# Optimization experiments

Measured on AMD Instinct MI355X. Metric: run time of the kernel, lower is better.

Reference implementation:

```python
import jax, jax.numpy as jnp
import numpy as np
import math

N_HEAD = 16
HEAD_DIM = 64
BASE = 10000.0

def setup_inputs() -> dict:
    key = jax.random.key(0)
    k1, k2, k3, k4 = jax.random.split(key, 4)
    B, T, C = 2, 2048, 1024
    x = jax.random.normal(k1, (B, T, C), dtype=jnp.float32)
    w_attn = jax.random.normal(k2, (3 * C, C), dtype=jnp.float32) * 0.02
    w_proj = jax.random.normal(k3, (C, C), dtype=jnp.float32) * 0.02
    delta = jax.random.normal(k4, (N_HEAD, HEAD_DIM), dtype=jnp.float32) * 0.5
    return {"x": x, "w_attn": w_attn, "w_proj": w_proj, "delta": delta}

def reference(x, w_attn, w_proj, delta):
    B, T, C = x.shape
    H, D = N_HEAD, HEAD_DIM
    # qkv projection (nn.Linear, no bias): x @ W^T
    qkv = jnp.einsum('btc,ec->bte', x, w_attn)
    q, k, v = jnp.split(qkv, 3, axis=-1)
    q = q.reshape(B, T, H, D).transpose(0, 2, 1, 3)  # (B,H,T,D)
    k = k.reshape(B, T, H, D).transpose(0, 2, 1, 3)
    v = v.reshape(B, T, H, D).transpose(0, 2, 1, 3)
    # PoPE: d frequencies per head
    inv_freq = 1.0 / (BASE ** (jnp.arange(D, dtype=jnp.float32) / D))  # (D,)
    t = jnp.arange(T, dtype=jnp.float32)
    freqs = t[:, None] * inv_freq[None, :]            # (T,D)
    cos_pos = jnp.cos(freqs)[None, None]              # (1,1,T,D)
    sin_pos = jnp.sin(freqs)[None, None]
    mu_q = jax.nn.softplus(q)
    mu_k = jax.nn.softplus(k)
    d = jnp.clip(delta, -2.0 * math.pi, 0.0)          # (H,D)
    cos_d = jnp.cos(d)[None, :, None, :]              # (1,H,1,D)
    sin_d = jnp.sin(d)[None, :, None, :]
    q_real = mu_q * cos_pos
    q_imag = mu_q * sin_pos
    k_real = mu_k * (cos_pos * cos_d - sin_pos * sin_d)
    k_imag = mu_k * (sin_pos * cos_d + cos_pos * sin_d)
    scale = 1.0 / math.sqrt(D)
    att = (jnp.einsum('bhtd,bhsd->bhts', q_real, k_real)
           + jnp.einsum('bhtd,bhsd->bhts', q_imag, k_imag)) * scale
    causal = jnp.tril(jnp.ones((T, T), dtype=bool))
    att = jnp.where(causal[None, None], att, -jnp.inf)
    att = jax.nn.softmax(att, axis=-1)
    y = jnp.einsum('bhts,bhsd->bhtd', att, v)
    y = y.transpose(0, 2, 1, 3).reshape(B, T, C)
    return jnp.einsum('btc,ec->bte', y, w_proj)
```

## Files before the change

kernel.cpp:

```cpp
#include <hip/hip_runtime.h>
#include <math.h>

typedef short s16x8 __attribute__((ext_vector_type(8)));
typedef float f32x4 __attribute__((ext_vector_type(4)));
typedef float f32x16 __attribute__((ext_vector_type(16)));
typedef unsigned short u16;

#define B_ 2
#define T_ 2048
#define HN_ 16

__device__ __forceinline__ u16 f2bf(float f) {
  union { float f; unsigned u; } v; v.f = f;
  unsigned r = v.u + 0x7FFFu + ((v.u >> 16) & 1u);
  return (u16)(r >> 16);
}
__device__ __forceinline__ float bf2f(u16 b) {
  union { unsigned u; float f; } v; v.u = ((unsigned)b) << 16;
  return v.f;
}
__device__ __forceinline__ float softplus_f(float v) {
  return fmaxf(v, 0.f) + __logf(1.f + __expf(-fabsf(v)));
}
__device__ __forceinline__ f32x4 mfma16(s16x8 a, s16x8 b, f32x4 c) {
  return __builtin_amdgcn_mfma_f32_16x16x32_bf16(a, b, c, 0, 0, 0);
}
__device__ __forceinline__ f32x16 mfma32(s16x8 a, s16x8 b, f32x16 c) {
  return __builtin_amdgcn_mfma_f32_32x32x16_bf16(a, b, c, 0, 0, 0);
}
__device__ __forceinline__ void gload16(void* lds, const void* g) {
  __builtin_amdgcn_global_load_lds(
      (const __attribute__((address_space(1))) unsigned int*)g,
      (__attribute__((address_space(3))) unsigned int*)lds, 16, 0, 0);
}
__device__ __forceinline__ unsigned cvtpk(float lo, float hi) {
  unsigned r;
  asm("v_cvt_pk_bf16_f32 %0, %1, %2" : "=v"(r) : "v"(lo), "v"(hi));
  return r;
}

__device__ __constant__ unsigned char QTC[72][3] = {
  {15,0,64},{15,1,65},{15,2,66},{15,3,67},{15,4,68},{15,5,69},{15,6,70},{15,7,71},
  {14,0,56},{14,1,57},{14,2,58},{14,3,59},{14,4,60},{14,5,61},{14,6,62},{14,7,63},
  {13,0,49},{13,1,50},{13,2,51},{13,3,52},{13,4,53},{13,5,54},{13,6,55},
  {12,0,42},{12,1,43},{12,2,44},{12,3,45},{12,4,46},{12,5,47},{12,6,48},
  {11,0,36},{11,1,37},{11,2,38},{11,3,39},{11,4,40},{11,5,41},
  {10,0,30},{10,1,31},{10,2,32},{10,3,33},{10,4,34},{10,5,35},
  {9,0,25},{9,1,26},{9,2,27},{9,3,28},{9,4,29},
  {8,0,20},{8,1,21},{8,2,22},{8,3,23},{8,4,24},
  {7,0,16},{7,1,17},{7,2,18},{7,3,19},
  {6,0,12},{6,1,13},{6,2,14},{6,3,15},
  {5,0,9},{5,1,10},{5,2,11},
  {4,0,6},{4,1,7},{4,2,8},
  {3,0,4},{3,1,5},
  {2,0,2},{2,1,3},
  {1,0,1},
  {0,0,0}
};
__device__ __constant__ unsigned char OFFT[16] =
  {0,1,2,4,6,9,12,16,20,25,30,36,42,49,56,64};

__global__ __launch_bounds__(256) void conv_swz(
    const float* __restrict__ in, u16* __restrict__ out, int nchunks)
{
  int c = blockIdx.x * 256 + threadIdx.x;
  if (c >= nchunks) return;
  int row = c >> 7, cc = c & 127;
  int ks = cc >> 3, ch = cc & 7;
  const float4* src = (const float4*)(in + ((size_t)row << 10) + (cc << 3));
  float4 a = src[0], b = src[1];
  s16x8 o;
  o[0] = (short)f2bf(a.x); o[1] = (short)f2bf(a.y);
  o[2] = (short)f2bf(a.z); o[3] = (short)f2bf(a.w);
  o[4] = (short)f2bf(b.x); o[5] = (short)f2bf(b.y);
  o[6] = (short)f2bf(b.z); o[7] = (short)f2bf(b.w);
  *(s16x8*)(out + ((size_t)row << 10) + (ks << 6) + ((ch ^ (row & 7)) << 3)) = o;
}

__global__ __launch_bounds__(256) void build_tables(
    float* __restrict__ postab, float* __restrict__ dtab,
    const float* __restrict__ delta)
{
  int idx = blockIdx.x * 256 + threadIdx.x;
  int t = idx >> 6, d = idx & 63;
  float invf = powf(10000.f, -(float)d * (1.0f / 64.0f));
  float ang = (float)t * invf;
  float sp, cp;
  sincosf(ang, &sp, &cp);
  postab[idx * 2 + 0] = cp;
  postab[idx * 2 + 1] = sp;
  if (idx < HN_ * 64) {
    float dl = delta[idx];
    dl = fminf(fmaxf(dl, -6.2831853071795865f), 0.f);
    float sd, cd;
    sincosf(dl, &sd, &cd);
    dtab[idx * 2 + 0] = cd;
    dtab[idx * 2 + 1] = sd;
  }
}

template<int OUTK>
__global__ __launch_bounds__(256) void gemm_nt_mfma(
    const u16* __restrict__ A, const u16* __restrict__ Bw,
    void* __restrict__ Cout, int N)
{
  __shared__ u16 As[128 * 64];
  __shared__ u16 Bs[128 * 64];
  const int tid = threadIdx.x;
  const int w = tid >> 6, l = tid & 63, g = l >> 4;
  const int bm = blockIdx.y * 128, bn = blockIdx.x * 128;
  const int wr = w >> 1, wc = w & 1;
  const int K = 1024;

  const f32x4 zero = {0.f, 0.f, 0.f, 0.f};
  f32x4 acc[4][4];
  #pragma unroll
  for (int mt = 0; mt < 4; ++mt)
    #pragma unroll
    for (int nt = 0; nt < 4; ++nt) acc[mt][nt] = zero;

  for (int kt = 0; kt < K; kt += 64) {
    __syncthreads();
    #pragma unroll
    for (int j = 0; j < 4; ++j) {
      int cid = (j * 4 + w) * 64 + l;
      int row = cid >> 3, cc = cid & 7;
      gload16(As + ((j * 4 + w) << 9), A  + (size_t)(bm + row) * K + kt + cc * 8);
      gload16(Bs + ((j * 4 + w) << 9), Bw + (size_t)(bn + row) * K + kt + cc * 8);
    }
    __syncthreads();
    #pragma unroll
    for (int ks = 0; ks < 2; ++ks) {
      s16x8 af[4], bfr[4];
      #pragma unroll
      for (int mt = 0; mt < 4; ++mt) {
        int rr = wr * 64 + mt * 16 + (l & 15);
        af[mt] = *(const s16x8*)(As + rr * 64 + (((ks * 4 + g) ^ (rr & 7)) << 3));
      }
      #pragma unroll
      for (int nt = 0; nt < 4; ++nt) {
        int rr = wc * 64 + nt * 16 + (l & 15);
        bfr[nt] = *(const s16x8*)(Bs + rr * 64 + (((ks * 4 + g) ^ (rr & 7)) << 3));
      }
      #pragma unroll
      for (int mt = 0; mt < 4; ++mt)
        #pragma unroll
        for (int nt = 0; nt < 4; ++nt)
          acc[mt][nt] = mfma16(af[mt], bfr[nt], acc[mt][nt]);
    }
  }

  #pragma unroll
  for (int mt = 0; mt < 4; ++mt)
    #pragma unroll
    for (int nt = 0; nt < 4; ++nt)
      #pragma unroll
      for (int r = 0; r < 4; ++r) {
        int row = bm + wr * 64 + mt * 16 + g * 4 + r;
        int col = bn + wc * 64 + nt * 16 + (l & 15);
        if (OUTK == 0)
          ((u16*)Cout)[(size_t)row * N + col] = f2bf(acc[mt][nt][r]);
        else
          ((float*)Cout)[(size_t)row * N + col] = acc[mt][nt][r];
      }
}

__global__ __launch_bounds__(256) void pope_prep(
    const u16* __restrict__ qkvb, const float* __restrict__ postab,
    const float* __restrict__ dtab, u16* __restrict__ Kp, u16* __restrict__ Vtp,
    u16* __restrict__ Qp, float* __restrict__ qn, int* __restrict__ knmaxI)
{
  __shared__ u16 Vs[64][72];
  __shared__ float knsh[64];
  const int tb = blockIdx.x, h = blockIdx.y, b = blockIdx.z;
  const int t0 = tb * 64, tid = threadIdx.x;
  const int tl = tid >> 2, j = tid & 3, d0 = j * 16;
  const int t = t0 + tl;
  const size_t bh = (size_t)b * HN_ + h;
  const size_t qrow = (size_t)(b * T_ + t) * 3072 + h * 64;
  const float2* pt = (const float2*)postab + (size_t)t * 64 + d0;

  float kss = 0.f;
  {
    s16x8 k0 = *(const s16x8*)(qkvb + qrow + 1024 + d0);
    s16x8 k1 = *(const s16x8*)(qkvb + qrow + 1024 + d0 + 8);
    const float2* dt = (const float2*)dtab + h * 64 + d0;
    s16x8 r0, r1, i0, i1;
    #pragma unroll
    for (int i = 0; i < 8; ++i) {
      float mu = softplus_f(bf2f((u16)k0[i]));
      kss += mu * mu;
      float2 cs = pt[i]; float2 dc = dt[i];
      r0[i] = (short)f2bf(mu * (cs.x * dc.x - cs.y * dc.y));
      i0[i] = (short)f2bf(mu * (cs.y * dc.x + cs.x * dc.y));
    }
    #pragma unroll
    for (int i = 0; i < 8; ++i) {
      float mu = softplus_f(bf2f((u16)k1[i]));
      kss += mu * mu;
      float2 cs = pt[8 + i]; float2 dc = dt[8 + i];
      r1[i] = (short)f2bf(mu * (cs.x * dc.x - cs.y * dc.y));
      i1[i] = (short)f2bf(mu * (cs.y * dc.x + cs.x * dc.y));
    }
    u16* Krow = Kp + (bh * T_ + t) * 128;
    int sw = t & 7;
    int c0 = d0 >> 3;
    *(s16x8*)(Krow + ((c0 ^ sw) << 3))       = r0;
    *(s16x8*)(Krow + (((c0 + 1) ^ sw) << 3)) = r1;
    *(s16x8*)(Krow + (((c0 + 8) ^ sw) << 3)) = i0;
    *(s16x8*)(Krow + (((c0 + 9) ^ sw) << 3)) = i1;
  }
  kss += __shfl_xor(kss, 1);
  kss += __shfl_xor(kss, 2);
  if (j == 0) knsh[tl] = kss;

  float qss = 0.f;
  {
    s16x8 q0 = *(const s16x8*)(qkvb + qrow + d0);
    s16x8 q1 = *(const s16x8*)(qkvb + qrow + d0 + 8);
    s16x8 r0, r1, i0, i1;
    #pragma unroll
    for (int i = 0; i < 8; ++i) {
      float mu = softplus_f(bf2f((u16)q0[i]));
      qss += mu * mu;
      float2 cs = pt[i];
      r0[i] = (short)f2bf(mu * cs.x);
      i0[i] = (short)f2bf(mu * cs.y);
    }
    #pragma unroll
    for (int i = 0; i < 8; ++i) {
      float mu = softplus_f(bf2f((u16)q1[i]));
      qss += mu * mu;
      float2 cs = pt[8 + i];
      r1[i] = (short)f2bf(mu * cs.x);
      i1[i] = (short)f2bf(mu * cs.y);
    }
    u16* Qrow = Qp + (bh * T_ + t) * 128;
    *(s16x8*)(Qrow + d0)          = r0;
    *(s16x8*)(Qrow + d0 + 8)      = r1;
    *(s16x8*)(Qrow + 64 + d0)     = i0;
    *(s16x8*)(Qrow + 64 + d0 + 8) = i1;
  }
  qss += __shfl_xor(qss, 1);
  qss += __shfl_xor(qss, 2);
  if (j == 0) qn[bh * T_ + t] = sqrtf(qss);

  {
    s16x8 v0 = *(const s16x8*)(qkvb + qrow + 2048 + d0);
    s16x8 v1 = *(const s16x8*)(qkvb + qrow + 2048 + d0 + 8);
    *(s16x8*)(&Vs[tl][d0])     = v0;
    *(s16x8*)(&Vs[tl][d0 + 8]) = v1;
  }
  __syncthreads();
  if (tid == 0) {
    float mx = 0.f;
    #pragma unroll
    for (int i = 0; i < 64; ++i) mx = fmaxf(mx, knsh[i]);
    atomicMax(knmaxI + bh, __float_as_int(sqrtf(mx)));
  }
  {
    const int d = tid >> 2, jj = tid & 3, ts0 = jj * 16;
    u16* Vrow = Vtp + (bh * 64 + d) * T_;
    int swd = d & 7;
    s16x8 o0, o1;
    #pragma unroll
    for (int i = 0; i < 8; ++i) {
      o0[i] = (short)Vs[ts0 + i][d];
      o1[i] = (short)Vs[ts0 + 8 + i][d];
    }
    int cc0 = ts0 >> 3;
    *(s16x8*)(Vrow + t0 + ((cc0 ^ swd) << 3))       = o0;
    *(s16x8*)(Vrow + t0 + (((cc0 + 1) ^ swd) << 3)) = o1;
  }
}

__global__ __launch_bounds__(256) void attn_split(
    const u16* __restrict__ Qp, const u16* __restrict__ Kp,
    const u16* __restrict__ Vtp, const float* __restrict__ qn,
    const int* __restrict__ knmaxI, u16* __restrict__ po, float* __restrict__ pl)
{
  const int xcd = (int)blockIdx.x & 7;
  const int idx = (int)blockIdx.x >> 3;
  const int bh = xcd + 8 * (idx / 72);
  const int w72 = idx % 72;
  const int qt = QTC[w72][0], c = QTC[w72][1];
  const int slot = bh * 72 + QTC[w72][2];

  __shared__ u16 smem[12288];
  u16* Ks  = smem;
  u16* Vts = smem + 8192;
  const int tid = threadIdx.x, w = tid >> 6, l = tid & 63;
  const int hi = l >> 5, ln = l & 31;

  const int kbeg = c * 256;
  const int kend0 = (qt + 1) * 128;
  const int kend = kend0 < kbeg + 256 ? kend0 : kbeg + 256;
  const int ntile = (kend - kbeg) >> 6;

  const float LS = 0.125f * 1.4426950408889634f;
  const u16* Kpb = Kp + (size_t)bh * T_ * 128;
  const u16* Vtb = Vtp + (size_t)bh * 64 * T_;

  const int q = qt * 128 + w * 32 + ln;
  s16x8 qf[8];
  {
    const u16* qrp = Qp + ((size_t)bh * T_ + q) * 128;
    #pragma unroll
    for (int ks = 0; ks < 8; ++ks)
      qf[ks] = *(const s16x8*)(qrp + ks * 16 + hi * 8);
  }
  const float knm = __int_as_float(knmaxI[bh]);
  const float m = LS * qn[(size_t)bh * T_ + q] * knm;

  const f32x16 zero16 = {0.f,0.f,0.f,0.f,0.f,0.f,0.f,0.f,
                         0.f,0.f,0.f,0.f,0.f,0.f,0.f,0.f};
  f32x16 o0 = zero16, o1 = zero16;
  float lsum = 0.f;
  const int qminw = qt * 128 + w * 32;

  for (int ti = 0; ti < ntile; ++ti) {
    const int s0 = kbeg + ti * 64;
    __syncthreads();
    #pragma unroll
    for (int jj = 0; jj < 4; ++jj) {
      int cid = (jj * 4 + w) * 64 + l;
      int row = cid >> 4, cc = cid & 15;
      gload16(Ks + ((jj * 4 + w) << 9), Kpb + (size_t)(s0 + row) * 128 + cc * 8);
    }
    #pragma unroll
    for (int jj = 0; jj < 2; ++jj) {
      int cid = (jj * 4 + w) * 64 + l;
      int row = cid >> 3, cc = cid & 7;
      gload16(Vts + ((jj * 4 + w) << 9), Vtb + (size_t)row * T_ + s0 + cc * 8);
    }
    __syncthreads();

    if (s0 <= qminw + 31) {
      const bool needmask = (s0 + 63) > qminw;

      f32x16 sacc0 = zero16, sacc1 = zero16;
      __builtin_amdgcn_s_setprio(1);
      #pragma unroll
      for (int ks = 0; ks < 8; ++ks) {
        int r0_ = ln, r1_ = 32 + ln;
        s16x8 kf0 = *(const s16x8*)(Ks + r0_ * 128 + (((2 * ks + hi) ^ (r0_ & 7)) << 3));
        s16x8 kf1 = *(const s16x8*)(Ks + r1_ * 128 + (((2 * ks + hi) ^ (r1_ & 7)) << 3));
        sacc0 = mfma32(kf0, qf[ks], sacc0);
        sacc1 = mfma32(kf1, qf[ks], sacc1);
      }
      __builtin_amdgcn_s_setprio(0);

      if (needmask) {
        #pragma unroll
        for (int jj = 0; jj < 16; ++jj) {
          int sg = s0 + (jj & 3) + 8 * (jj >> 2) + 4 * hi;
          if (sg > q)      sacc0[jj] = -3e38f;
          if (sg + 32 > q) sacc1[jj] = -3e38f;
        }
      }
      float rs = 0.f;
      #pragma unroll
      for (int jj = 0; jj < 16; ++jj) {
        float p0 = exp2f(fmaf(sacc0[jj], LS, -m));
        float p1 = exp2f(fmaf(sacc1[jj], LS, -m));
        sacc0[jj] = p0; sacc1[jj] = p1;
        rs += p0 + p1;
      }
      lsum += rs;

      s16x8 pa[4];
      #pragma unroll
      for (int ks = 0; ks < 4; ++ks) {
        const int bb = (ks & 1) * 8;
        unsigned pk01, pk23, pk45, pk67;
        if (ks < 2) {
          pk01 = cvtpk(sacc0[bb + 0], sacc0[bb + 1]);
          pk23 = cvtpk(sacc0[bb + 2], sacc0[bb + 3]);
          pk45 = cvtpk(sacc0[bb + 4], sacc0[bb + 5]);
          pk67 = cvtpk(sacc0[bb + 6], sacc0[bb + 7]);
        } else {
          pk01 = cvtpk(sacc1[bb + 0], sacc1[bb + 1]);
          pk23 = cvtpk(sacc1[bb + 2], sacc1[bb + 3]);
          pk45 = cvtpk(sacc1[bb + 4], sacc1[bb + 5]);
          pk67 = cvtpk(sacc1[bb + 6], sacc1[bb + 7]);
        }
        unsigned sv0 = hi ? pk01 : pk45;
        unsigned sv1 = hi ? pk23 : pk67;
        unsigned r0 = (unsigned)__shfl_xor((int)sv0, 32);
        unsigned r1 = (unsigned)__shfl_xor((int)sv1, 32);
        union { unsigned u[4]; s16x8 v; } pu;
        pu.u[0] = hi ? r0 : pk01;
        pu.u[1] = hi ? r1 : pk23;
        pu.u[2] = hi ? pk45 : r0;
        pu.u[3] = hi ? pk67 : r1;
        pa[ks] = pu.v;
      }

      __builtin_amdgcn_s_setprio(1);
      #pragma unroll
      for (int ks = 0; ks < 4; ++ks) {
        int rd0 = ln, rd1 = 32 + ln;
        s16x8 vb0 = *(const s16x8*)(Vts + rd0 * 64 + (((2 * ks + hi) ^ (rd0 & 7)) << 3));
        s16x8 vb1 = *(const s16x8*)(Vts + rd1 * 64 + (((2 * ks + hi) ^ (rd1 & 7)) << 3));
        o0 = mfma32(pa[ks], vb0, o0);
        o1 = mfma32(pa[ks], vb1, o1);
      }
      __builtin_amdgcn_s_setprio(0);
    }
  }

  lsum += __shfl_xor(lsum, 32);
  u16* pob = po + (size_t)slot * 8192;
  #pragma unroll
  for (int jj = 0; jj < 16; ++jj) {
    int row = w * 32 + 4 * hi + (jj & 3) + 8 * (jj >> 2);
    pob[row * 64 + ln]      = f2bf(o0[jj]);
    pob[row * 64 + 32 + ln] = f2bf(o1[jj]);
  }
  if (hi == 0)
    pl[(size_t)slot * 128 + w * 32 + ln] = lsum;
}

__global__ __launch_bounds__(256) void attn_combine(
    const u16* __restrict__ po, const float* __restrict__ pl,
    u16* __restrict__ yb)
{
  const int qt = blockIdx.x, bh = blockIdx.y;
  const int b = bh >> 4, h = bh & 15;
  const int nch = (qt + 2) >> 1;
  const int base = bh * 72 + OFFT[qt];
  const int t = threadIdx.x;
  const int row = t >> 1, d0 = (t & 1) * 32;

  float acc[32];
  #pragma unroll
  for (int i = 0; i < 32; ++i) acc[i] = 0.f;
  float ls = 0.f;
  for (int c = 0; c < nch; ++c) {
    const u16* pr = po + (size_t)(base + c) * 8192 + row * 64 + d0;
    #pragma unroll
    for (int v = 0; v < 4; ++v) {
      s16x8 x = *(const s16x8*)(pr + v * 8);
      #pragma unroll
      for (int i = 0; i < 8; ++i) acc[v * 8 + i] += bf2f((u16)x[i]);
    }
    ls += pl[(size_t)(base + c) * 128 + row];
  }
  float inv = 1.f / ls;
  int qrow = qt * 128 + row;
  size_t rb = (size_t)(b * T_ + qrow) * 1024 + h * 64;
  #pragma unroll
  for (int v = 0; v < 4; ++v) {
    int ch = ((d0 >> 3) + v) ^ (qrow & 7);
    s16x8 o;
    #pragma unroll
    for (int i = 0; i < 8; ++i) o[i] = (short)f2bf(acc[v * 8 + i] * inv);
    *(s16x8*)(yb + rb + (ch << 3)) = o;
  }
}

extern "C" void kernel_launch(void* const* d_in, const int* in_sizes, int n_in,
                              void* d_out, int out_size, void* d_ws, size_t ws_size,
                              hipStream_t stream)
{
  const float* x      = (const float*)d_in[0];
  const float* w_attn = (const float*)d_in[1];
  const float* w_proj = (const float*)d_in[2];
  const float* delta  = (const float*)d_in[3];
  float* out = (float*)d_out;

  char* p = (char*)d_ws;
  u16* qkvb   = (u16*)p;
  u16* xb     = (u16*)(p + (size_t)4096 * 3072 * 2);
  u16* wab    = (u16*)(p + (size_t)4096 * 3072 * 2 + (size_t)4096 * 1024 * 2);
  u16* po     = (u16*)p;
  p += (size_t)(4096 * 3072 + 4096 * 1024 + 3072 * 1024) * 2;
  u16* wpb    = (u16*)p;  p += (size_t)1024 * 1024 * 2;
  u16* yb     = (u16*)p;  p += (size_t)4096 * 1024 * 2;
  u16* Kp     = (u16*)p;  p += (size_t)B_ * HN_ * T_ * 128 * 2;
  u16* Vtp    = (u16*)p;  p += (size_t)B_ * HN_ * 64 * T_ * 2;
  u16* Qp     = (u16*)p;  p += (size_t)B_ * HN_ * T_ * 128 * 2;
  float* postab = (float*)p; p += (size_t)T_ * 64 * 2 * 4;
  float* dtab   = (float*)p; p += (size_t)HN_ * 64 * 2 * 4;
  float* qn     = (float*)p; p += (size_t)B_ * HN_ * T_ * 4;
  float* pl     = (float*)p; p += (size_t)2304 * 128 * 4;
  int*   knmaxI = (int*)p;   p += 32 * 4;

  conv_swz<<<(4096 * 128) / 256, 256, 0, stream>>>(x, xb, 4096 * 128);
  conv_swz<<<(3072 * 128) / 256, 256, 0, stream>>>(w_attn, wab, 3072 * 128);
  conv_swz<<<(1024 * 128) / 256, 256, 0, stream>>>(w_proj, wpb, 1024 * 128);
  build_tables<<<(T_ * 64) / 256, 256, 0, stream>>>(postab, dtab, delta);
  hipMemsetAsync(knmaxI, 0, 32 * 4, stream);

  gemm_nt_mfma<0><<<dim3(3072 / 128, 4096 / 128), 256, 0, stream>>>(xb, wab, qkvb, 3072);
  pope_prep<<<dim3(T_ / 64, HN_, B_), 256, 0, stream>>>(qkvb, postab, dtab, Kp, Vtp,
                                                        Qp, qn, knmaxI);
  attn_split<<<dim3(2304), 256, 0, stream>>>(Qp, Kp, Vtp, qn, knmaxI, po, pl);
  attn_combine<<<dim3(16, 32), 256, 0, stream>>>(po, pl, yb);
  gemm_nt_mfma<1><<<dim3(1024 / 128, 4096 / 128), 256, 0, stream>>>(yb, wpb, out, 1024);
}
```

Before: 169.9 us.

## Double-buffer K/V tiles in attention, use permlane32 swap, XCD-aware combine order

The attention split kernel now double-buffers the K and V^T shared-memory tiles. It issues async global-to-LDS loads for the next tile before computing on the current one and uses partial vmcnt waits with raw barriers. The shuffle-based exchange of P fragments between half-waves is replaced by v_permlane32_swap instructions. The combine kernel switches to a 1D grid with XCD-aware block mapping that schedules the longest query tiles first. Shared memory use doubles, which may reduce occupancy, and the hand-placed waitcnt counts must match the number of outstanding loads.

Result: faster. 163.8 us (-3.6%).

```diff
diff --git a/kernel.cpp b/kernel.cpp
--- a/kernel.cpp
+++ b/kernel.cpp
@@ -286,9 +286,7 @@
   const int qt = QTC[w72][0], c = QTC[w72][1];
   const int slot = bh * 72 + QTC[w72][2];
 
-  __shared__ u16 smem[12288];
-  u16* Ks  = smem;
-  u16* Vts = smem + 8192;
+  __shared__ u16 smem[2][12288];
   const int tid = threadIdx.x, w = tid >> 6, l = tid & 63;
   const int hi = l >> 5, ln = l & 31;
 
@@ -301,6 +299,23 @@
   const u16* Kpb = Kp + (size_t)bh * T_ * 128;
   const u16* Vtb = Vtp + (size_t)bh * 64 * T_;
 
+  auto STAGE = [&](int buf, int s0) {
+    u16* Kd = smem[buf];
+    u16* Vd = smem[buf] + 8192;
+    #pragma unroll
+    for (int jj = 0; jj < 4; ++jj) {
+      int cid = (jj * 4 + w) * 64 + l;
+      int row = cid >> 4, cc = cid & 15;
+      gload16(Kd + ((jj * 4 + w) << 9), Kpb + (size_t)(s0 + row) * 128 + cc * 8);
+    }
+    #pragma unroll
+    for (int jj = 0; jj < 2; ++jj) {
+      int cid = (jj * 4 + w) * 64 + l;
+      int row = cid >> 3, cc = cid & 7;
+      gload16(Vd + ((jj * 4 + w) << 9), Vtb + (size_t)row * T_ + s0 + cc * 8);
+    }
+  };
+
   const int q = qt * 128 + w * 32 + ln;
   s16x8 qf[8];
   {
@@ -311,6 +326,8 @@
   }
   const float knm = __int_as_float(knmaxI[bh]);
   const float m = LS * qn[(size_t)bh * T_ + q] * knm;
+
+  asm volatile("s_waitcnt vmcnt(0)" ::: "memory");
 
   const f32x16 zero16 = {0.f,0.f,0.f,0.f,0.f,0.f,0.f,0.f,
                          0.f,0.f,0.f,0.f,0.f,0.f,0.f,0.f};
@@ -318,22 +335,22 @@
   float lsum = 0.f;
   const int qminw = qt * 128 + w * 32;
 
+  STAGE(0, kbeg);
+  int cur = 0;
+
   for (int ti = 0; ti < ntile; ++ti) {
     const int s0 = kbeg + ti * 64;
-    __syncthreads();
-    #pragma unroll
-    for (int jj = 0; jj < 4; ++jj) {
-      int cid = (jj * 4 + w) * 64 + l;
-      int row = cid >> 4, cc = cid & 15;
-      gload16(Ks + ((jj * 4 + w) << 9), Kpb + (size_t)(s0 + row) * 128 + cc * 8);
-    }
-    #pragma unroll
-    for (int jj = 0; jj < 2; ++jj) {
-      int cid = (jj * 4 + w) * 64 + l;
-      int row = cid >> 3, cc = cid & 7;
-      gload16(Vts + ((jj * 4 + w) << 9), Vtb + (size_t)row * T_ + s0 + cc * 8);
-    }
-    __syncthreads();
+    if (ti + 1 < ntile) {
+      STAGE(cur ^ 1, s0 + 64);
+      asm volatile("s_waitcnt vmcnt(6)" ::: "memory");
+    } else {
+      asm volatile("s_waitcnt vmcnt(0)" ::: "memory");
+    }
+    __builtin_amdgcn_s_barrier();
+    __builtin_amdgcn_sched_barrier(0);
+
+    const u16* Ks  = smem[cur];
+    const u16* Vts = smem[cur] + 8192;
 
     if (s0 <= qminw + 31) {
       const bool needmask = (s0 + 63) > qminw;
@@ -372,27 +389,22 @@
       #pragma unroll
       for (int ks = 0; ks < 4; ++ks) {
         const int bb = (ks & 1) * 8;
-        unsigned pk01, pk23, pk45, pk67;
+        unsigned a0, a1, b0v, b1v;
         if (ks < 2) {
-          pk01 = cvtpk(sacc0[bb + 0], sacc0[bb + 1]);
-          pk23 = cvtpk(sacc0[bb + 2], sacc0[bb + 3]);
-          pk45 = cvtpk(sacc0[bb + 4], sacc0[bb + 5]);
-          pk67 = cvtpk(sacc0[bb + 6], sacc0[bb + 7]);
+          a0  = cvtpk(sacc0[bb + 0], sacc0[bb + 1]);
+          a1  = cvtpk(sacc0[bb + 2], sacc0[bb + 3]);
+          b0v = cvtpk(sacc0[bb + 4], sacc0[bb + 5]);
+          b1v = cvtpk(sacc0[bb + 6], sacc0[bb + 7]);
         } else {
-          pk01 = cvtpk(sacc1[bb + 0], sacc1[bb + 1]);
-          pk23 = cvtpk(sacc1[bb + 2], sacc1[bb + 3]);
-          pk45 = cvtpk(sacc1[bb + 4], sacc1[bb + 5]);
-          pk67 = cvtpk(sacc1[bb + 6], sacc1[bb + 7]);
+          a0  = cvtpk(sacc1[bb + 0], sacc1[bb + 1]);
+          a1  = cvtpk(sacc1[bb + 2], sacc1[bb + 3]);
+          b0v = cvtpk(sacc1[bb + 4], sacc1[bb + 5]);
+          b1v = cvtpk(sacc1[bb + 6], sacc1[bb + 7]);
         }
-        unsigned sv0 = hi ? pk01 : pk45;
-        unsigned sv1 = hi ? pk23 : pk67;
-        unsigned r0 = (unsigned)__shfl_xor((int)sv0, 32);
-        unsigned r1 = (unsigned)__shfl_xor((int)sv1, 32);
+        asm("v_permlane32_swap_b32 %0, %1" : "+v"(a0), "+v"(b0v));
+        asm("v_permlane32_swap_b32 %0, %1" : "+v"(a1), "+v"(b1v));
         union { unsigned u[4]; s16x8 v; } pu;
-        pu.u[0] = hi ? r0 : pk01;
-        pu.u[1] = hi ? r1 : pk23;
-        pu.u[2] = hi ? pk45 : r0;
-        pu.u[3] = hi ? pk67 : r1;
+        pu.u[0] = a0; pu.u[1] = a1; pu.u[2] = b0v; pu.u[3] = b1v;
         pa[ks] = pu.v;
       }
 
@@ -407,6 +419,8 @@
       }
       __builtin_amdgcn_s_setprio(0);
     }
+    __builtin_amdgcn_s_barrier();
+    cur ^= 1;
   }
 
   lsum += __shfl_xor(lsum, 32);
@@ -425,7 +439,10 @@
     const u16* __restrict__ po, const float* __restrict__ pl,
     u16* __restrict__ yb)
 {
-  const int qt = blockIdx.x, bh = blockIdx.y;
+  const int xcd = (int)blockIdx.x & 7;
+  const int i = (int)blockIdx.x >> 3;
+  const int bh = xcd + 8 * (i & 3);
+  const int qt = 15 - (i >> 2);
   const int b = bh >> 4, h = bh & 15;
   const int nch = (qt + 2) >> 1;
   const int base = bh * 72 + OFFT[qt];
@@ -434,7 +451,7 @@
 
   float acc[32];
   #pragma unroll
-  for (int i = 0; i < 32; ++i) acc[i] = 0.f;
+  for (int i2 = 0; i2 < 32; ++i2) acc[i2] = 0.f;
   float ls = 0.f;
   for (int c = 0; c < nch; ++c) {
     const u16* pr = po + (size_t)(base + c) * 8192 + row * 64 + d0;
@@ -442,7 +459,7 @@
     for (int v = 0; v < 4; ++v) {
       s16x8 x = *(const s16x8*)(pr + v * 8);
       #pragma unroll
-      for (int i = 0; i < 8; ++i) acc[v * 8 + i] += bf2f((u16)x[i]);
+      for (int i2 = 0; i2 < 8; ++i2) acc[v * 8 + i2] += bf2f((u16)x[i2]);
     }
     ls += pl[(size_t)(base + c) * 128 + row];
   }
@@ -454,7 +471,7 @@
     int ch = ((d0 >> 3) + v) ^ (qrow & 7);
     s16x8 o;
     #pragma unroll
-    for (int i = 0; i < 8; ++i) o[i] = (short)f2bf(acc[v * 8 + i] * inv);
+    for (int i2 = 0; i2 < 8; ++i2) o[i2] = (short)f2bf(acc[v * 8 + i2] * inv);
     *(s16x8*)(yb + rb + (ch << 3)) = o;
   }
 }
@@ -496,6 +513,6 @@
   pope_prep<<<dim3(T_ / 64, HN_, B_), 256, 0, stream>>>(qkvb, postab, dtab, Kp, Vtp,
                                                         Qp, qn, knmaxI);
   attn_split<<<dim3(2304), 256, 0, stream>>>(Qp, Kp, Vtp, qn, knmaxI, po, pl);
-  attn_combine<<<dim3(16, 32), 256, 0, stream>>>(po, pl, yb);
+  attn_combine<<<dim3(512), 256, 0, stream>>>(po, pl, yb);
   gemm_nt_mfma<1><<<dim3(1024 / 128, 4096 / 128), 256, 0, stream>>>(yb, wpb, out, 1024);
 }
```
